# Optimization experiments

Hardware: AMD Instinct MI355X
Metric: run time of the kernel (lower is better)

The kernel has to match this reference:

```python
import jax, jax.numpy as jnp
import numpy as np

B, N, C_IN = 4, 2048, 64
HID, HEADS, NQ = 128, 4, 16
D = HID // HEADS  # per-head dim = 32
NEG_SLOPE = 0.2
MASK_VAL = -1e9


def setup_inputs() -> dict:
    key = jax.random.key(0)
    ks = jax.random.split(key, 8)
    x = jax.random.normal(ks[0], (B, N, C_IN), dtype=jnp.float32)
    adj = jax.random.randint(ks[1], (N, N), 0, 2, dtype=jnp.int32)
    # lin_in: Linear(in_channels, hidden_dim)
    W_in = jax.random.normal(ks[2], (C_IN, HID), dtype=jnp.float32) / np.sqrt(C_IN)
    b_in = jnp.zeros((HID,), dtype=jnp.float32)
    # attention vectors [1, heads, d]
    att_src = jax.random.normal(ks[3], (1, HEADS, D), dtype=jnp.float32) * 0.1
    att_dst = jax.random.normal(ks[4], (1, HEADS, D), dtype=jnp.float32) * 0.1
    # output_head: Linear(num_nodes*hidden_dim, num_qubits)
    W_out = jax.random.normal(ks[5], (N * HID, NQ), dtype=jnp.float32) / np.sqrt(N * HID)
    b_out = jnp.zeros((NQ,), dtype=jnp.float32)
    return {"x": x, "adj": adj, "W_in": W_in, "b_in": b_in,
            "att_src": att_src, "att_dst": att_dst,
            "W_out": W_out, "b_out": b_out}


def reference(x, adj, W_in, b_in, att_src, att_dst, W_out, b_out):
    b, n, _ = x.shape
    h = (x @ W_in + b_in).reshape(b, n, HEADS, D)          # [B,N,H,D]
    alpha_src = jnp.sum(h * att_src, axis=-1)               # [B,N,H]
    alpha_dst = jnp.sum(h * att_dst, axis=-1)               # [B,N,H]
    # additive scores: score[b,i,j,h] = src[b,i,h] + dst[b,j,h]
    scores = alpha_src[:, :, None, :] + alpha_dst[:, None, :, :]  # [B,N,N,H]
    scores = jnp.where(scores >= 0, scores, NEG_SLOPE * scores)   # leaky relu
    mask = (adj == 0)[None, :, :, None]                     # [1,N,N,1]
    scores = jnp.where(mask, MASK_VAL, scores)
    alpha = jax.nn.softmax(scores, axis=2)                  # softmax over neighbors j
    # dropout p=0.0 (eval) -> identity
    out = jnp.einsum('bijh,bjhd->bihd', alpha, h)           # [B,N,H,D]
    out = out.reshape(b, n * HEADS * D)                     # [B, N*HID]
    return out @ W_out + b_out                              # [B, NQ]
```

## Files before the change

kernel.cpp:

```cpp
#include <hip/hip_runtime.h>
#include <math.h>

#define BB 4
#define NN 2048
#define CIN 64
#define HID 128
#define HEADS 4
#define NQ 16
#define KTOT (NN*HID)
#define LOG2E 1.44269504088896340736f
#define NEGBIG_BITS 0xC2C80000u
#define NSL 2

typedef __attribute__((ext_vector_type(8))) _Float16 half8;
typedef __attribute__((ext_vector_type(2))) _Float16 half2;
typedef __attribute__((ext_vector_type(4))) float f32x4;
typedef __attribute__((ext_vector_type(4))) unsigned uint4v;

#define GLDS16(g, l) __builtin_amdgcn_global_load_lds((const __attribute__((address_space(1))) unsigned int*)(g), (__attribute__((address_space(3))) unsigned int*)(l), 16, 0, 0)
#define GLDS4(g, l)  __builtin_amdgcn_global_load_lds((const __attribute__((address_space(1))) unsigned int*)(g), (__attribute__((address_space(3))) unsigned int*)(l), 4, 0, 0)

__global__ __launch_bounds__(256) void k_hidden(
    const float* __restrict__ x, const float* __restrict__ W_in,
    const float* __restrict__ b_in, const float* __restrict__ att_src,
    const float* __restrict__ att_dst, _Float16* __restrict__ hH,
    float* __restrict__ srcA, float* __restrict__ dstA)
{
    __shared__ float Wl[CIN * HID];
    __shared__ float xl[16][CIN];
    const int t = threadIdx.x;
    const int jj0 = blockIdx.x * 16;

    {
        const float4* Ws = (const float4*)W_in;
        float4* Wd = (float4*)Wl;
#pragma unroll
        for (int u = 0; u < 8; ++u) Wd[t + 256 * u] = Ws[t + 256 * u];
        ((float4*)&xl[0][0])[t] = ((const float4*)(x + (size_t)jj0 * CIN))[t];
    }
    __syncthreads();

    const int c = t & 127, rg = t >> 7;
    const int b = jj0 >> 11, j0 = (jj0 & (NN - 1)) + rg * 8;
    const int h = c >> 5;

    float acc[8];
    const float bc = b_in[c];
#pragma unroll
    for (int rr = 0; rr < 8; ++rr) acc[rr] = bc;

#pragma unroll
    for (int k4 = 0; k4 < CIN; k4 += 4) {
        const float w0 = Wl[(k4 + 0) * HID + c];
        const float w1 = Wl[(k4 + 1) * HID + c];
        const float w2 = Wl[(k4 + 2) * HID + c];
        const float w3 = Wl[(k4 + 3) * HID + c];
#pragma unroll
        for (int rr = 0; rr < 8; ++rr) {
            const float4 xv = *(const float4*)&xl[rg * 8 + rr][k4];
            acc[rr] = fmaf(xv.w, w3, fmaf(xv.z, w2, fmaf(xv.y, w1, fmaf(xv.x, w0, acc[rr]))));
        }
    }

    half8 hv;
#pragma unroll
    for (int rr = 0; rr < 8; ++rr) hv[rr] = (_Float16)acc[rr];
    *(half8*)(hH + (size_t)(b * HID + c) * NN + j0) = hv;

    const float as = att_src[c], ad = att_dst[c];
#pragma unroll
    for (int rr = 0; rr < 8; ++rr) {
        float vs = acc[rr] * as, vd = acc[rr] * ad;
#pragma unroll
        for (int m = 16; m >= 1; m >>= 1) {
            vs += __shfl_xor(vs, m, 64);
            vd += __shfl_xor(vd, m, 64);
        }
        if ((t & 31) == 0) {
            srcA[(size_t)(b * HEADS + h) * NN + j0 + rr] = vs * LOG2E;
            dstA[(size_t)(b * HEADS + h) * NN + j0 + rr] = vd * LOG2E;
        }
    }
}

__global__ __launch_bounds__(256) void k_adjb(const int* __restrict__ adj,
                                              unsigned* __restrict__ adjb,
                                              const float* __restrict__ b_out,
                                              float* __restrict__ dout)
{
    const int t = threadIdx.x;
    if (blockIdx.x == 0 && t < 64) dout[t] = b_out[t & 15];
    const int gid = blockIdx.x * 256 + t;
    const int lane = t & 63;
    const int4* p = (const int4*)(adj + (size_t)gid * 8);
    const int4 a = p[0], b = p[1];
    unsigned byte =
        (a.x != 0 ? 1u : 0u)  | (a.y != 0 ? 2u : 0u)  | (a.z != 0 ? 4u : 0u)  | (a.w != 0 ? 8u : 0u) |
        (b.x != 0 ? 16u : 0u) | (b.y != 0 ? 32u : 0u) | (b.z != 0 ? 64u : 0u) | (b.w != 0 ? 128u : 0u);
    unsigned u = byte | (((unsigned)__shfl_xor((int)byte, 1, 64)) << 8);
    u = u | (((unsigned)__shfl_xor((int)u, 2, 64)) << 16);
    if ((lane & 3) == 0) adjb[gid >> 2] = u;
}

__global__ __launch_bounds__(512, 4) void k_attn(
    const unsigned* __restrict__ adjb, const _Float16* __restrict__ hH,
    const float* __restrict__ srcA, const float* __restrict__ dstA,
    float* __restrict__ P, float* __restrict__ S)
{
    __shared__ __align__(16) char sm[2 * 16384 + 2 * 1024 + 2 * 256];

    const int t = threadIdx.x;
    const int lane = t & 63;
    const int w = t >> 6;
    const int h = w & 3;
    const int ih = w >> 2;
    const int bx = blockIdx.x;
    const int jh = bx >> 8;
    const int b = (bx >> 6) & 3;
    const int i0 = (bx & 63) * 32;
    const int jbase = jh * 1024;

    const int r16 = lane & 15;
    const int g = lane >> 4;
    const int sw = (r16 & 7) << 4;

    const float srci = srcA[(size_t)(b * HEADS + h) * NN + i0 + ih * 16 + r16];

    auto STAGE = [&](int cur, int n) {
        const int jt = jbase + n * 64;
        {
            const int d0 = t >> 3;
            const int j8a = (t & 7) ^ (d0 & 7);
            GLDS16(hH + ((size_t)(b * HID) + d0) * NN + jt + j8a * 8,
                   sm + cur * 16384 + w * 1024);
            const int d1 = 64 + (t >> 3);
            const int j8b = (t & 7) ^ (d1 & 7);
            GLDS16(hH + ((size_t)(b * HID) + d1) * NN + jt + j8b * 8,
                   sm + cur * 16384 + 8192 + w * 1024);
        }
        if (w == 0) {
            const int hh = lane >> 4, j4 = lane & 15;
            GLDS16(dstA + (size_t)(b * HEADS + hh) * NN + jt + j4 * 4,
                   sm + 32768 + cur * 1024);
        }
        if (w == 1) {
            const int row = lane >> 1, wd = lane & 1;
            GLDS4(adjb + (size_t)(i0 + row) * (NN / 32) + (jt >> 5) + wd,
                  sm + 34816 + cur * 256);
        }
    };

    f32x4 acc0 = {0.f, 0.f, 0.f, 0.f};
    f32x4 acc1 = {0.f, 0.f, 0.f, 0.f};
    f32x4 accS = {0.f, 0.f, 0.f, 0.f};
    const half8 ones = {(_Float16)1.f, (_Float16)1.f, (_Float16)1.f, (_Float16)1.f,
                        (_Float16)1.f, (_Float16)1.f, (_Float16)1.f, (_Float16)1.f};

    STAGE(0, 0);
    asm volatile("s_waitcnt vmcnt(0)" ::: "memory");
    __syncthreads();

    int cur = 0;
    for (int n = 0; n < 16; ++n) {
        if (n + 1 < 16) STAGE(cur ^ 1, n + 1);

        const uint2 aw = *(const uint2*)(sm + 34816 + cur * 256 + (ih * 16 + r16) * 8);
        const char* hb = sm + cur * 16384 + (h * 32 + r16) * 128;
        const char* db = sm + 32768 + cur * 1024 + h * 256;

#pragma unroll
        for (int jg = 0; jg < 2; ++jg) {
            const int cb = jg * 64 + g * 16;
            const half8 bb0 = *(const half8*)(hb + (cb ^ sw));
            const half8 bb1 = *(const half8*)(hb + 16 * 128 + (cb ^ sw));
            const float4 dv0 = *(const float4*)(db + jg * 128 + g * 32);
            const float4 dv1 = *(const float4*)(db + jg * 128 + g * 32 + 16);
            const unsigned bits = (jg ? aw.y : aw.x) >> (8 * g);
            const float dvv[8] = {dv0.x, dv0.y, dv0.z, dv0.w, dv1.x, dv1.y, dv1.z, dv1.w};
            float wv[8];
#pragma unroll
            for (int e = 0; e < 8; ++e) {
                float s = srci + dvv[e];
                s = fmaxf(s, 0.2f * s);
                const unsigned m = (unsigned)(((int)(bits << (31 - e))) >> 31);
                const unsigned su = __builtin_bit_cast(unsigned, s);
                wv[e] = __builtin_amdgcn_exp2f(
                    __builtin_bit_cast(float, (su & m) | (NEGBIG_BITS & ~m)));
            }
            uint4v uu;
            uu[0] = __builtin_bit_cast(unsigned, __builtin_amdgcn_cvt_pkrtz(wv[0], wv[1]));
            uu[1] = __builtin_bit_cast(unsigned, __builtin_amdgcn_cvt_pkrtz(wv[2], wv[3]));
            uu[2] = __builtin_bit_cast(unsigned, __builtin_amdgcn_cvt_pkrtz(wv[4], wv[5]));
            uu[3] = __builtin_bit_cast(unsigned, __builtin_amdgcn_cvt_pkrtz(wv[6], wv[7]));
            const half8 af = __builtin_bit_cast(half8, uu);
            acc0 = __builtin_amdgcn_mfma_f32_16x16x32_f16(af, bb0, acc0, 0, 0, 0);
            acc1 = __builtin_amdgcn_mfma_f32_16x16x32_f16(af, bb1, acc1, 0, 0, 0);
            accS = __builtin_amdgcn_mfma_f32_16x16x32_f16(af, ones, accS, 0, 0, 0);
        }

        asm volatile("s_waitcnt vmcnt(0)" ::: "memory");
        __syncthreads();
        cur ^= 1;
    }

    const size_t prow0 = (size_t)(jh * BB + b) * NN + i0 + ih * 16;
#pragma unroll
    for (int r = 0; r < 4; ++r) {
        const size_t row = prow0 + 4 * g + r;
        P[row * HID + h * 32 + r16]      = acc0[r];
        P[row * HID + h * 32 + 16 + r16] = acc1[r];
        if (r16 == 0) S[row * HEADS + h] = accS[r];
    }
}

__global__ __launch_bounds__(256) void k_proj(
    const float* __restrict__ P, const float* __restrict__ S,
    const float* __restrict__ W_out, float* __restrict__ dout)
{
    __shared__ float wlT[NQ][260];
    __shared__ float red[256];

    const int t = threadIdx.x;
    const int k0 = blockIdx.x * 256;

#pragma unroll
    for (int u = 0; u < 4; ++u) {
        const int flat = (u * 256 + t) * 4;
        const float4 wv = *(const float4*)(W_out + (size_t)k0 * NQ + flat);
        const int krel = flat >> 4;
        const int q0 = flat & 15;
        wlT[q0 + 0][krel] = wv.x;
        wlT[q0 + 1][krel] = wv.y;
        wlT[q0 + 2][krel] = wv.z;
        wlT[q0 + 3][krel] = wv.w;
    }
    __syncthreads();

    const int q = t & 15;
    const int b = (t >> 4) & 3;
    const int ks = (t >> 6) * 64;
    const int i = (k0 + ks) >> 7;

    const float* p0 = P + (size_t)b * KTOT + k0 + ks;
    const float* p1 = P + (size_t)(BB + b) * KTOT + k0 + ks;

    float acc = 0.f;
#pragma unroll
    for (int seg = 0; seg < 2; ++seg) {
        const int h = ((k0 + ks + seg * 32) >> 5) & 3;
        const float rs = S[((size_t)b * NN + i) * HEADS + h] +
                         S[((size_t)(BB + b) * NN + i) * HEADS + h];
        const float inv = __builtin_amdgcn_rcpf(rs);
#pragma unroll
        for (int k4 = 0; k4 < 8; ++k4) {
            const int kk = seg * 32 + k4 * 4;
            const float4 a0 = *(const float4*)(p0 + kk);
            const float4 a1 = *(const float4*)(p1 + kk);
            const float4 wq = *(const float4*)&wlT[q][ks + kk];
            acc = fmaf((a0.x + a1.x) * inv, wq.x, acc);
            acc = fmaf((a0.y + a1.y) * inv, wq.y, acc);
            acc = fmaf((a0.z + a1.z) * inv, wq.z, acc);
            acc = fmaf((a0.w + a1.w) * inv, wq.w, acc);
        }
    }

    red[t] = acc;
    __syncthreads();
    if (t < 64)
        atomicAdd(&dout[t], red[t] + red[t + 64] + red[t + 128] + red[t + 192]);
}

extern "C" void kernel_launch(void* const* d_in, const int* in_sizes, int n_in,
                              void* d_out, int out_size, void* d_ws, size_t ws_size,
                              hipStream_t stream)
{
    const float* x       = (const float*)d_in[0];
    const int*   adj     = (const int*)d_in[1];
    const float* W_in    = (const float*)d_in[2];
    const float* b_in    = (const float*)d_in[3];
    const float* att_src = (const float*)d_in[4];
    const float* att_dst = (const float*)d_in[5];
    const float* W_out   = (const float*)d_in[6];
    const float* b_out   = (const float*)d_in[7];
    float* out = (float*)d_out;

    float* P    = (float*)d_ws;
    float* S    = P + (size_t)NSL * BB * KTOT;
    float* srcA = S + (size_t)NSL * BB * NN * HEADS;
    float* dstA = srcA + (size_t)BB * HEADS * NN;
    _Float16* hH = (_Float16*)(dstA + (size_t)BB * HEADS * NN);
    unsigned* adjbw = (unsigned*)((char*)hH + sizeof(_Float16) * (size_t)BB * KTOT);

    k_hidden<<<BB * NN / 16, 256, 0, stream>>>(x, W_in, b_in, att_src, att_dst, hH, srcA, dstA);
    k_adjb<<<NN * NN / 8 / 256, 256, 0, stream>>>(adj, adjbw, b_out, out);
    k_attn<<<NSL * BB * (NN / 32), 512, 0, stream>>>(adjbw, hH, srcA, dstA, P, S);
    k_proj<<<KTOT / 256, 256, 0, stream>>>(P, S, W_out, out);
}
```

Before: 75.08 us.

## Give each wave a private LDS buffer and drop block barriers in attention kernel

Restructures k_attn so each 64-thread wave stages only its own head's hidden slice into a private double-buffered LDS region. This removes every __syncthreads from the main loop. Adjacency words and dst scores are now read straight from global memory per lane instead of being staged in shared memory. Blocks shrink to 256 threads and the grid doubles, splitting the i half-tiles across blocks. The hidden tiles are no longer shared between the two i-halves, so global and L2 traffic for them roughly doubles, and there are more direct global loads inside the loop.

Result: slower. 77.76 us (+3.6%).

```diff
diff --git a/kernel.cpp b/kernel.cpp
--- a/kernel.cpp
+++ b/kernel.cpp
@@ -18,7 +18,6 @@
 typedef __attribute__((ext_vector_type(4))) unsigned uint4v;
 
 #define GLDS16(g, l) __builtin_amdgcn_global_load_lds((const __attribute__((address_space(1))) unsigned int*)(g), (__attribute__((address_space(3))) unsigned int*)(l), 16, 0, 0)
-#define GLDS4(g, l)  __builtin_amdgcn_global_load_lds((const __attribute__((address_space(1))) unsigned int*)(g), (__attribute__((address_space(3))) unsigned int*)(l), 4, 0, 0)
 
 __global__ __launch_bounds__(256) void k_hidden(
     const float* __restrict__ x, const float* __restrict__ W_in,
@@ -102,52 +101,44 @@
     if ((lane & 3) == 0) adjb[gid >> 2] = u;
 }
 
-__global__ __launch_bounds__(512, 4) void k_attn(
+__global__ __launch_bounds__(256, 4) void k_attn(
     const unsigned* __restrict__ adjb, const _Float16* __restrict__ hH,
     const float* __restrict__ srcA, const float* __restrict__ dstA,
     float* __restrict__ P, float* __restrict__ S)
 {
-    __shared__ __align__(16) char sm[2 * 16384 + 2 * 1024 + 2 * 256];
+    __shared__ __align__(16) char sm[4 * 8192];
 
     const int t = threadIdx.x;
     const int lane = t & 63;
     const int w = t >> 6;
-    const int h = w & 3;
-    const int ih = w >> 2;
+    const int h = w;
     const int bx = blockIdx.x;
-    const int jh = bx >> 8;
-    const int b = (bx >> 6) & 3;
-    const int i0 = (bx & 63) * 32;
+    const int ih = bx & 1;
+    const int it = (bx >> 1) & 63;
+    const int b = (bx >> 7) & 3;
+    const int jh = bx >> 9;
+    const int i0 = it * 32;
     const int jbase = jh * 1024;
 
     const int r16 = lane & 15;
     const int g = lane >> 4;
-    const int sw = (r16 & 7) << 4;
-
+    const int sw16 = (r16 & 7) << 4;
+
+    char* mybuf = sm + w * 8192;
+    const _Float16* hrow = hH + ((size_t)(b * HID) + h * 32) * NN;
     const float srci = srcA[(size_t)(b * HEADS + h) * NN + i0 + ih * 16 + r16];
-
-    auto STAGE = [&](int cur, int n) {
+    const uint2* adjr = (const uint2*)(adjb + (size_t)(i0 + ih * 16 + r16) * (NN / 32)) + (jbase >> 6);
+    const float4* dstt = (const float4*)(dstA + (size_t)(b * HEADS + h) * NN + jbase);
+
+    const int srow = lane >> 3;
+    const int sj8 = (lane & 7) ^ srow;
+    auto STAGE = [&](int buf, int n) {
         const int jt = jbase + n * 64;
-        {
-            const int d0 = t >> 3;
-            const int j8a = (t & 7) ^ (d0 & 7);
-            GLDS16(hH + ((size_t)(b * HID) + d0) * NN + jt + j8a * 8,
-                   sm + cur * 16384 + w * 1024);
-            const int d1 = 64 + (t >> 3);
-            const int j8b = (t & 7) ^ (d1 & 7);
-            GLDS16(hH + ((size_t)(b * HID) + d1) * NN + jt + j8b * 8,
-                   sm + cur * 16384 + 8192 + w * 1024);
-        }
-        if (w == 0) {
-            const int hh = lane >> 4, j4 = lane & 15;
-            GLDS16(dstA + (size_t)(b * HEADS + hh) * NN + jt + j4 * 4,
-                   sm + 32768 + cur * 1024);
-        }
-        if (w == 1) {
-            const int row = lane >> 1, wd = lane & 1;
-            GLDS4(adjb + (size_t)(i0 + row) * (NN / 32) + (jt >> 5) + wd,
-                  sm + 34816 + cur * 256);
-        }
+        const _Float16* gsrc = hrow + (size_t)srow * NN + jt + sj8 * 8;
+        char* ldst = mybuf + buf * 4096;
+#pragma unroll
+        for (int u = 0; u < 4; ++u)
+            GLDS16(gsrc + (size_t)(u * 8) * NN, ldst + u * 1024);
     };
 
     f32x4 acc0 = {0.f, 0.f, 0.f, 0.f};
@@ -158,23 +149,22 @@
 
     STAGE(0, 0);
     asm volatile("s_waitcnt vmcnt(0)" ::: "memory");
-    __syncthreads();
-
-    int cur = 0;
+
+    int buf = 0;
+#pragma unroll 1
     for (int n = 0; n < 16; ++n) {
-        if (n + 1 < 16) STAGE(cur ^ 1, n + 1);
-
-        const uint2 aw = *(const uint2*)(sm + 34816 + cur * 256 + (ih * 16 + r16) * 8);
-        const char* hb = sm + cur * 16384 + (h * 32 + r16) * 128;
-        const char* db = sm + 32768 + cur * 1024 + h * 256;
+        if (n + 1 < 16) STAGE(buf ^ 1, n + 1);
+
+        const uint2 aw = adjr[n];
+        const char* hb = mybuf + buf * 4096;
 
 #pragma unroll
         for (int jg = 0; jg < 2; ++jg) {
             const int cb = jg * 64 + g * 16;
-            const half8 bb0 = *(const half8*)(hb + (cb ^ sw));
-            const half8 bb1 = *(const half8*)(hb + 16 * 128 + (cb ^ sw));
-            const float4 dv0 = *(const float4*)(db + jg * 128 + g * 32);
-            const float4 dv1 = *(const float4*)(db + jg * 128 + g * 32 + 16);
+            const half8 bb0 = *(const half8*)(hb + r16 * 128 + (cb ^ sw16));
+            const half8 bb1 = *(const half8*)(hb + (16 + r16) * 128 + (cb ^ sw16));
+            const float4 dv0 = dstt[n * 16 + jg * 8 + g * 2];
+            const float4 dv1 = dstt[n * 16 + jg * 8 + g * 2 + 1];
             const unsigned bits = (jg ? aw.y : aw.x) >> (8 * g);
             const float dvv[8] = {dv0.x, dv0.y, dv0.z, dv0.w, dv1.x, dv1.y, dv1.z, dv1.w};
             float wv[8];
@@ -199,8 +189,7 @@
         }
 
         asm volatile("s_waitcnt vmcnt(0)" ::: "memory");
-        __syncthreads();
-        cur ^= 1;
+        buf ^= 1;
     }
 
     const size_t prow0 = (size_t)(jh * BB + b) * NN + i0 + ih * 16;
@@ -293,6 +282,6 @@
 
     k_hidden<<<BB * NN / 16, 256, 0, stream>>>(x, W_in, b_in, att_src, att_dst, hH, srcA, dstA);
     k_adjb<<<NN * NN / 8 / 256, 256, 0, stream>>>(adj, adjbw, b_out, out);
-    k_attn<<<NSL * BB * (NN / 32), 512, 0, stream>>>(adjbw, hH, srcA, dstA, P, S);
+    k_attn<<<NSL * BB * (NN / 32) * 2, 256, 0, stream>>>(adjbw, hH, srcA, dstA, P, S);
     k_proj<<<KTOT / 256, 256, 0, stream>>>(P, S, W_out, out);
 }
```
